# Kernel optimization log

Hardware: AMD Instinct MI355X
Metric: run time of the kernel (lower is better)

The kernel has to match this reference:

```python
import jax, jax.numpy as jnp
import numpy as np

B, S, D = 8, 2048, 512

def setup_inputs() -> dict:
    key = jax.random.key(0)
    ks = jax.random.split(key, 7)
    scale = 1.0 / np.sqrt(D)
    return {
        "x": jax.random.normal(ks[0], (B, S, D), dtype=jnp.float32),
        "Wq": jax.random.normal(ks[1], (D, D), dtype=jnp.float32) * scale,
        "bq": jax.random.normal(ks[2], (D,), dtype=jnp.float32) * 0.01,
        "Wk": jax.random.normal(ks[3], (D, D), dtype=jnp.float32) * scale,
        "bk": jax.random.normal(ks[4], (D,), dtype=jnp.float32) * 0.01,
        "Wv": jax.random.normal(ks[5], (D, D), dtype=jnp.float32) * scale,
        "bv": jax.random.normal(ks[6], (D,), dtype=jnp.float32) * 0.01,
    }

def reference(x, Wq, bq, Wk, bk, Wv, bv):
    # Q/K/V projections: [B,S,D] @ [D,D]
    q = jnp.einsum('bsd,de->bse', x, Wq) + bq
    k = jnp.einsum('bsd,de->bse', x, Wk) + bk
    v = jnp.einsum('bsd,de->bse', x, Wv) + bv
    # NOTE: original module has NO 1/sqrt(d) scaling
    scores = jnp.einsum('bqd,bkd->bqk', q, k)          # [B,S,S]
    attn = jax.nn.softmax(scores, axis=-1)
    return jnp.einsum('bqk,bkd->bqd', attn, v)         # [B,S,D]
```

## Files before the change

kernel.cpp:

```cpp
#include <hip/hip_runtime.h>
#include <hip/hip_fp16.h>


typedef unsigned short u16;
typedef unsigned int u32;
typedef __attribute__((ext_vector_type(8))) _Float16 f16x8;
typedef __attribute__((ext_vector_type(16))) float f32x16;

#define S_LEN 2048
#define D_DIM 512
#define B_N 8

__device__ __forceinline__ u16 f2bf(float f) {
    u32 u = __float_as_uint(f);
    u32 r = u + 0x7FFFu + ((u >> 16) & 1u);
    return (u16)(r >> 16);
}
__device__ __forceinline__ float bf2f(u16 h) {
    return __uint_as_float((u32)h << 16);
}
__device__ __forceinline__ u16 f2h(float f) {
    _Float16 h = (_Float16)f;
    return *(u16*)&h;
}
__device__ __forceinline__ void gl16(const u16* g, u16* l) {
    __builtin_amdgcn_global_load_lds(
        (const __attribute__((address_space(1))) void*)g,
        (__attribute__((address_space(3))) void*)l, 16, 0, 0);
}
__device__ __forceinline__ f32x16 mfma16(f16x8 a, f16x8 b, f32x16 c) {
    return __builtin_amdgcn_mfma_f32_32x32x16_f16(a, b, c, 0, 0, 0);
}

__global__ void detect_k(const u16* __restrict__ x, int* __restrict__ flag)
{
    int t = threadIdx.x;
    u16 u = x[2 * t];
    int e = (u >> 7) & 0xFF;
    int sane = (e == 0) || (e >= 110 && e <= 140);
    unsigned long long b = __ballot(sane);
    if (t == 0) *flag = (__popcll(b) >= 32) ? 1 : 0;
}

__global__ __launch_bounds__(256) void cvt_x(
    const void* __restrict__ X, u16* __restrict__ xf,
    const int* __restrict__ flagp)
{
    const size_t i4 = ((size_t)blockIdx.x * 256 + threadIdx.x) * 4;
    float f[4];
    if (*flagp) {
        ushort4 u = *(const ushort4*)((const u16*)X + i4);
        f[0] = bf2f(u.x); f[1] = bf2f(u.y); f[2] = bf2f(u.z); f[3] = bf2f(u.w);
    } else {
        float4 ff = *(const float4*)((const float*)X + i4);
        f[0] = ff.x; f[1] = ff.y; f[2] = ff.z; f[3] = ff.w;
    }
    ushort4 h;
    h.x = f2h(f[0]); h.y = f2h(f[1]); h.z = f2h(f[2]); h.w = f2h(f[3]);
    *(ushort4*)(xf + i4) = h;
}

__global__ __launch_bounds__(256) void pack_w(
    const void* __restrict__ Wq, const void* __restrict__ Wk, const void* __restrict__ Wv,
    u16* __restrict__ WT, const int* __restrict__ flagp)
{
    const int k = blockIdx.x;
    const int n = blockIdx.y * 256 + threadIdx.x;
    const void* W = n < 512 ? Wq : n < 1024 ? Wk : Wv;
    const int nc = n & 511;
    float f = *flagp ? bf2f(((const u16*)W)[(size_t)k * 512 + nc])
                     : ((const float*)W)[(size_t)k * 512 + nc];
    WT[(size_t)n * 512 + k] = f2h(f);
}

__global__ void pack_bias(
    const void* __restrict__ bq, const void* __restrict__ bk, const void* __restrict__ bv,
    float* __restrict__ bcat, const int* __restrict__ flagp)
{
    const int t = blockIdx.x * 256 + threadIdx.x;
    const void* b = t < 512 ? bq : t < 1024 ? bk : bv;
    const int i = t & 511;
    bcat[t] = *flagp ? bf2f(((const u16*)b)[i]) : ((const float*)b)[i];
}

template <int EPI>
__global__ __launch_bounds__(256) void gemm_f16(
    const u16* __restrict__ A_, const u16* __restrict__ B_,
    void* __restrict__ Cp, const float* __restrict__ biasf,
    u16* __restrict__ Oq, u16* __restrict__ Ok, u16* __restrict__ OvT,
    const int* __restrict__ flagp,
    int K, int lda, int ldb, int ldc, long sA, long sB, long sC, long cbase)
{
    const int tid = threadIdx.x;
    const int lane = tid & 63, wav = tid >> 6;
    const int l31 = lane & 31, lh = lane >> 5;

    int bx, by, bz;
    if constexpr (EPI != 2) {
        const int gx = gridDim.x, gy = gridDim.y;
        const int total = gx * gy * gridDim.z;
        const int chunk = total >> 3;
        int lin = (blockIdx.z * gy + blockIdx.y) * gx + blockIdx.x;
        lin = (lin & 7) * chunk + (lin >> 3);
        bx = lin % gx;
        by = (lin / gx) % gy;
        bz = lin / (gx * gy);
    } else {
        bx = blockIdx.x; by = blockIdx.y; bz = blockIdx.z;
    }

    const int m0 = by * 128, n0 = bx * 128;
    const int bm = (wav >> 1) * 64, bn = (wav & 1) * 64;

    const u16* A = A_ + (size_t)bz * sA;
    const u16* B = B_ + (size_t)bz * sB;

    __shared__ __align__(16) u16 sh[16384];
    u16* As = sh;
    u16* Bs = sh + 8192;

    const int r0 = tid >> 3;
    const int c0 = ((tid & 7) ^ (r0 & 7)) * 8;
    size_t aoff[4], boff[4];
#pragma unroll
    for (int j = 0; j < 4; j++) {
        aoff[j] = (size_t)(m0 + r0 + j * 32) * lda + c0;
        boff[j] = (size_t)(n0 + r0 + j * 32) * ldb + c0;
    }
    const int g7 = l31 & 7;
    const int rowA0 = (bm + l31) * 64, rowA1 = (bm + 32 + l31) * 64;
    const int rowB0 = (bn + l31) * 64, rowB1 = (bn + 32 + l31) * 64;

    f32x16 acc[2][2];
#pragma unroll
    for (int i = 0; i < 2; i++)
#pragma unroll
        for (int j = 0; j < 2; j++)
#pragma unroll
            for (int r = 0; r < 16; r++) acc[i][j][r] = 0.f;

    for (int k0 = 0; k0 < K; k0 += 64) {
#pragma unroll
        for (int j = 0; j < 4; j++) {
            gl16(A + aoff[j] + k0, As + j * 2048 + wav * 512);
            gl16(B + boff[j] + k0, Bs + j * 2048 + wav * 512);
        }
        __syncthreads();

#pragma unroll
        for (int h = 0; h < 4; h++) {
            const int so = ((h * 2 + lh) ^ g7) * 8;
            f16x8 af[2], bfr[2];
            af[0] = *(const f16x8*)&As[rowA0 + so];
            af[1] = *(const f16x8*)&As[rowA1 + so];
            bfr[0] = *(const f16x8*)&Bs[rowB0 + so];
            bfr[1] = *(const f16x8*)&Bs[rowB1 + so];
#pragma unroll
            for (int i = 0; i < 2; i++)
#pragma unroll
                for (int j = 0; j < 2; j++)
                    acc[i][j] = mfma16(af[i], bfr[j], acc[i][j]);
        }
        __syncthreads();
    }

    if (EPI == 2) {
        const int mode = bx >> 2;
        if (mode == 2) {
#pragma unroll
            for (int it = 0; it < 2; it++)
#pragma unroll
                for (int jt = 0; jt < 2; jt++) {
                    const int lc = bn + jt * 32 + l31;
                    const float badd = biasf[n0 + lc];
#pragma unroll
                    for (int r = 0; r < 16; r++) {
                        const int row = bm + it * 32 + (r & 3) + 8 * (r >> 2) + 4 * lh;
                        sh[lc * 128 + (row ^ ((lc & 15) << 3))] =
                            f2h(acc[it][jt][r] + badd);
                    }
                }
            __syncthreads();
            const int vbase = n0 - 1024;
#pragma unroll
            for (int p = 0; p < 8; p++) {
                const int q = p * 256 + tid;
                const int lc = q >> 4, ch = q & 15;
                const int g = ch ^ (lc & 15);
                f16x8 val = *(const f16x8*)&sh[lc * 128 + g * 8];
                *(f16x8*)&OvT[(size_t)(vbase + lc) * 16384 + m0 + ch * 8] = val;
            }
        } else {
#pragma unroll
            for (int it = 0; it < 2; it++)
#pragma unroll
                for (int jt = 0; jt < 2; jt++) {
                    const int gcol = n0 + bn + jt * 32 + l31;
                    const int lcol = gcol & 511;
                    const float badd = biasf[gcol];
#pragma unroll
                    for (int r = 0; r < 16; r++) {
                        const int row = m0 + bm + it * 32 + (r & 3) + 8 * (r >> 2) + 4 * lh;
                        const float v = acc[it][jt][r] + badd;
                        if (mode == 0) Oq[(size_t)row * 512 + lcol] = f2h(v);
                        else           Ok[(size_t)row * 512 + lcol] = f2h(v);
                    }
                }
        }
    } else if (EPI == 0) {
        float* Cf = (float*)Cp;
        const long coff = (long)bz * sC;
#pragma unroll
        for (int it = 0; it < 2; it++)
#pragma unroll
            for (int jt = 0; jt < 2; jt++) {
                const int col = n0 + bn + jt * 32 + l31;
#pragma unroll
                for (int r = 0; r < 16; r++) {
                    const int row = m0 + bm + it * 32 + (r & 3) + 8 * (r >> 2) + 4 * lh;
                    Cf[(size_t)(coff + (long)row * ldc + col)] = acc[it][jt][r];
                }
            }
    } else {
        const int isbf = *flagp;
        float* Cf = (float*)Cp;
        u16* Cb = (u16*)Cp;
        const long coff = cbase + (long)bz * sC;
#pragma unroll
        for (int it = 0; it < 2; it++)
#pragma unroll
            for (int jt = 0; jt < 2; jt++) {
                const int col = n0 + bn + jt * 32 + l31;
#pragma unroll
                for (int r = 0; r < 16; r++) {
                    const int row = m0 + bm + it * 32 + (r & 3) + 8 * (r >> 2) + 4 * lh;
                    const size_t idx = (size_t)(coff + (long)row * ldc + col);
                    if (isbf) Cb[idx] = f2bf(acc[it][jt][r]);
                    else Cf[idx] = acc[it][jt][r];
                }
            }
    }
}

__global__ __launch_bounds__(256) void softmax_k(float* __restrict__ sc)
{
    float* srow = sc + (size_t)blockIdx.x * S_LEN;
    const int tid = threadIdx.x;

    float4 a = ((const float4*)srow)[tid];
    float4 b = ((const float4*)srow)[256 + tid];

    float m = fmaxf(fmaxf(fmaxf(a.x, a.y), fmaxf(a.z, a.w)),
                    fmaxf(fmaxf(b.x, b.y), fmaxf(b.z, b.w)));
#pragma unroll
    for (int off = 32; off > 0; off >>= 1) m = fmaxf(m, __shfl_down(m, off));

    __shared__ float redm[4], reds[4];
    if ((tid & 63) == 0) redm[tid >> 6] = m;
    __syncthreads();
    m = fmaxf(fmaxf(redm[0], redm[1]), fmaxf(redm[2], redm[3]));

    a.x = __expf(a.x - m); a.y = __expf(a.y - m);
    a.z = __expf(a.z - m); a.w = __expf(a.w - m);
    b.x = __expf(b.x - m); b.y = __expf(b.y - m);
    b.z = __expf(b.z - m); b.w = __expf(b.w - m);
    float s = a.x + a.y + a.z + a.w + b.x + b.y + b.z + b.w;
#pragma unroll
    for (int off = 32; off > 0; off >>= 1) s += __shfl_down(s, off);
    if ((tid & 63) == 0) reds[tid >> 6] = s;
    __syncthreads();
    s = reds[0] + reds[1] + reds[2] + reds[3];

    const float inv = 1.0f / s;
    ushort4 pa, pb;
    pa.x = f2h(a.x * inv); pa.y = f2h(a.y * inv);
    pa.z = f2h(a.z * inv); pa.w = f2h(a.w * inv);
    pb.x = f2h(b.x * inv); pb.y = f2h(b.y * inv);
    pb.z = f2h(b.z * inv); pb.w = f2h(b.w * inv);
    ((ushort4*)srow)[tid] = pa;
    ((ushort4*)srow)[256 + tid] = pb;
}

extern "C" void kernel_launch(void* const* d_in, const int* in_sizes, int n_in,
                              void* d_out, int out_size, void* d_ws, size_t ws_size,
                              hipStream_t stream)
{
    const void* x  = d_in[0];
    const void* Wq = d_in[1]; const void* bq = d_in[2];
    const void* Wk = d_in[3]; const void* bk = d_in[4];
    const void* Wv = d_in[5]; const void* bv = d_in[6];

    const int S = S_LEN, D = D_DIM;
    const long SD = (long)S * D;

    char* w = (char*)d_ws;
    int*   flag = (int*)w;
    u16*   WT   = (u16*)(w + 1024);
    float* bcat = (float*)(w + 1573888);
    u16*   xf   = (u16*)(w + 1580032);
    u16*   qf   = (u16*)(w + 18357248);
    u16*   kf   = (u16*)(w + 35134464);
    u16*   vT   = (u16*)(w + 51911680);
    float* scA  = (float*)(w + 68688896);

    const size_t avail = ws_size > 68688896ull ? ws_size - 68688896ull : 0;
    const size_t perb = (size_t)S * S * 4;
    const int c = avail >= 8 * perb ? 8 : avail >= 4 * perb ? 4 : avail >= 2 * perb ? 2 : 1;

    dim3 blk(256);

    detect_k<<<1, 64, 0, stream>>>((const u16*)x, flag);
    cvt_x<<<8192, blk, 0, stream>>>(x, xf, flag);
    pack_w<<<dim3(512, 6), blk, 0, stream>>>(Wq, Wk, Wv, WT, flag);
    pack_bias<<<6, blk, 0, stream>>>(bq, bk, bv, bcat, flag);

    gemm_f16<2><<<dim3(12, 128, 1), blk, 0, stream>>>(
        xf, WT, nullptr, bcat, qf, kf, vT, flag,
        512, 512, 512, 0, 0, 0, 0, 0);

    for (int cb = 0; cb < B_N; cb += c) {
        const size_t off = (size_t)cb * SD;
        gemm_f16<0><<<dim3(16, 16, c), blk, 0, stream>>>(
            qf + off, kf + off, scA, nullptr, nullptr, nullptr, nullptr, flag,
            512, 512, 512, S, SD, SD, (long)S * S, 0);
        softmax_k<<<c * S, blk, 0, stream>>>(scA);
        gemm_f16<1><<<dim3(4, 16, c), blk, 0, stream>>>(
            (const u16*)scA, vT + (size_t)cb * S, d_out, nullptr,
            nullptr, nullptr, nullptr, flag,
            S, 2 * S, B_N * S, D, 2ll * S * S, S, SD, (long)cb * SD);
    }
}
```

Baseline: 274.7 us.

## Replace P·V GEMM with 512-thread triple-buffered 16x16x32 MFMA kernel

Adds a dedicated gemm8pv kernel for the attention-probabilities times V product. It uses 256x128 tiles with 8 waves, triple-buffered LDS stages filled by global_load_lds, and 16x16x32 MFMAs. Global loads are interleaved with the MFMA phases, with explicit waitcnt/barriers and setprio. This is meant to hide load latency and raise MFMA throughput for the largest GEMM. In exchange it uses much more LDS with one block per CU, and fewer blocks (4x8xc), which may limit occupancy.

```diff
diff --git a/kernel.cpp b/kernel.cpp
--- a/kernel.cpp
+++ b/kernel.cpp
@@ -6,6 +6,7 @@
 typedef unsigned int u32;
 typedef __attribute__((ext_vector_type(8))) _Float16 f16x8;
 typedef __attribute__((ext_vector_type(16))) float f32x16;
+typedef __attribute__((ext_vector_type(4))) float f32x4;
 
 #define S_LEN 2048
 #define D_DIM 512
@@ -30,6 +31,9 @@
 }
 __device__ __forceinline__ f32x16 mfma16(f16x8 a, f16x8 b, f32x16 c) {
     return __builtin_amdgcn_mfma_f32_32x32x16_f16(a, b, c, 0, 0, 0);
+}
+__device__ __forceinline__ f32x4 mfma16q(f16x8 a, f16x8 b, f32x4 c) {
+    return __builtin_amdgcn_mfma_f32_16x16x32_f16(a, b, c, 0, 0, 0);
 }
 
 __global__ void detect_k(const u16* __restrict__ x, int* __restrict__ flag)
@@ -207,7 +211,7 @@
                     }
                 }
         }
-    } else if (EPI == 0) {
+    } else {
         float* Cf = (float*)Cp;
         const long coff = (long)bz * sC;
 #pragma unroll
@@ -221,23 +225,164 @@
                     Cf[(size_t)(coff + (long)row * ldc + col)] = acc[it][jt][r];
                 }
             }
-    } else {
-        const int isbf = *flagp;
-        float* Cf = (float*)Cp;
-        u16* Cb = (u16*)Cp;
-        const long coff = cbase + (long)bz * sC;
-#pragma unroll
-        for (int it = 0; it < 2; it++)
-#pragma unroll
-            for (int jt = 0; jt < 2; jt++) {
-                const int col = n0 + bn + jt * 32 + l31;
-#pragma unroll
-                for (int r = 0; r < 16; r++) {
-                    const int row = m0 + bm + it * 32 + (r & 3) + 8 * (r >> 2) + 4 * lh;
-                    const size_t idx = (size_t)(coff + (long)row * ldc + col);
-                    if (isbf) Cb[idx] = f2bf(acc[it][jt][r]);
-                    else Cf[idx] = acc[it][jt][r];
+    }
+}
+
+__global__ __launch_bounds__(512, 1) void gemm8pv(
+    const u16* __restrict__ A_, const u16* __restrict__ B_,
+    void* __restrict__ Cp, const int* __restrict__ flagp,
+    int K, int lda, int ldb, int ldc, long sA, long sB, long sC, long cbase)
+{
+    const int tid = threadIdx.x;
+    const int lane = tid & 63;
+    const int wid = tid >> 6;
+    const int wm = wid >> 2;
+    const int wn = wid & 3;
+    const int l15 = lane & 15, lq = lane >> 4;
+    const int colB = wn * 32;
+
+    const int gx = gridDim.x, gy = gridDim.y;
+    const int total = gx * gy * gridDim.z;
+    const int chunk = total >> 3;
+    int lin = (blockIdx.z * gy + blockIdx.y) * gx + blockIdx.x;
+    lin = (lin & 7) * chunk + (lin >> 3);
+    const int bx = lin % gx;
+    const int by = (lin / gx) % gy;
+    const int bz = lin / (gx * gy);
+
+    const int m0 = by * 256, n0 = bx * 128;
+
+    const u16* A = A_ + (size_t)bz * sA;
+    const u16* B = B_ + (size_t)bz * sB;
+
+    __shared__ __align__(16) u16 As[3][256 * 64];
+    __shared__ __align__(16) u16 Bs[3][128 * 64];
+
+    const int r0 = tid >> 3;
+    const int c0 = ((tid & 7) ^ (r0 & 7)) * 8;
+    u32 aoffs[4], boffs[2];
+#pragma unroll
+    for (int j = 0; j < 4; j++)
+        aoffs[j] = (u32)((m0 + j * 64 + r0) * lda + c0);
+#pragma unroll
+    for (int j = 0; j < 2; j++)
+        boffs[j] = (u32)((n0 + j * 64 + r0) * ldb + c0);
+    const int stageDst = wid << 9;
+
+    const int nt = K >> 6;
+
+    f32x4 acc[8][2];
+#pragma unroll
+    for (int mi = 0; mi < 8; mi++)
+#pragma unroll
+        for (int nj = 0; nj < 2; nj++)
+#pragma unroll
+            for (int r = 0; r < 4; r++) acc[mi][nj][r] = 0.f;
+
+    auto stage6 = [&](u16* dA, u16* dB, int k0) {
+#pragma unroll
+        for (int j = 0; j < 4; j++)
+            gl16(A + aoffs[j] + k0, dA + (j << 12) + stageDst);
+#pragma unroll
+        for (int j = 0; j < 2; j++)
+            gl16(B + boffs[j] + k0, dB + (j << 12) + stageDst);
+    };
+    auto rdA = [&](const u16* buf, int p, int h, int ks) -> f16x8 {
+        const int row = (wm << 7) + (p << 5) + (h << 4) + l15;
+        const int off = (row << 6) + ((((ks << 2) + lq) ^ (row & 7)) << 3);
+        return *(const f16x8*)(buf + off);
+    };
+    auto rdB = [&](const u16* buf, int nj, int ks) -> f16x8 {
+        const int row = colB + (nj << 4) + l15;
+        const int off = (row << 6) + ((((ks << 2) + lq) ^ (row & 7)) << 3);
+        return *(const f16x8*)(buf + off);
+    };
+
+    stage6(As[0], Bs[0], 0);
+    stage6(As[1], Bs[1], 64);
+    asm volatile("s_waitcnt vmcnt(6)" ::: "memory");
+    __builtin_amdgcn_sched_barrier(0);
+    __builtin_amdgcn_s_barrier();
+
+    for (int tt = 0; tt < nt; tt++) {
+        const int bi = tt % 3, si = (tt + 2) % 3;
+        const u16* Ab = As[bi];
+        const u16* Bb = Bs[bi];
+        u16* dA = As[si];
+        u16* dB = Bs[si];
+        const bool doStage = (tt + 2 < nt);
+        const int k2 = (tt + 2) * 64;
+        f16x8 bfr[2][2];
+#pragma unroll
+        for (int p = 0; p < 4; p++) {
+            if (p == 0) {
+#pragma unroll
+                for (int nj = 0; nj < 2; nj++)
+#pragma unroll
+                    for (int ks = 0; ks < 2; ks++)
+                        bfr[nj][ks] = rdB(Bb, nj, ks);
+            }
+            f16x8 a[2][2];
+#pragma unroll
+            for (int h = 0; h < 2; h++)
+#pragma unroll
+                for (int ks = 0; ks < 2; ks++)
+                    a[h][ks] = rdA(Ab, p, h, ks);
+            if (doStage) {
+                if (p == 0) {
+                    gl16(A + aoffs[0] + k2, dA + stageDst);
+                    gl16(A + aoffs[1] + k2, dA + (1 << 12) + stageDst);
+                } else if (p == 1) {
+                    gl16(A + aoffs[2] + k2, dA + (2 << 12) + stageDst);
+                    gl16(A + aoffs[3] + k2, dA + (3 << 12) + stageDst);
+                } else if (p == 2) {
+                    gl16(B + boffs[0] + k2, dB + stageDst);
+                    gl16(B + boffs[1] + k2, dB + (1 << 12) + stageDst);
                 }
+            }
+            if (p == 3) {
+                asm volatile("s_waitcnt lgkmcnt(0)" ::: "memory");
+                __builtin_amdgcn_sched_barrier(0);
+            }
+            __builtin_amdgcn_s_barrier();
+            __builtin_amdgcn_s_setprio(1);
+#pragma unroll
+            for (int h = 0; h < 2; h++)
+#pragma unroll
+                for (int nj = 0; nj < 2; nj++)
+#pragma unroll
+                    for (int ks = 0; ks < 2; ks++)
+                        acc[2 * p + h][nj] =
+                            mfma16q(a[h][ks], bfr[nj][ks], acc[2 * p + h][nj]);
+            __builtin_amdgcn_s_setprio(0);
+            if (p < 3) {
+                __builtin_amdgcn_s_barrier();
+            } else if (tt + 1 < nt) {
+                if (tt + 2 < nt)
+                    asm volatile("s_waitcnt vmcnt(6)" ::: "memory");
+                else
+                    asm volatile("s_waitcnt vmcnt(0)" ::: "memory");
+                __builtin_amdgcn_sched_barrier(0);
+                __builtin_amdgcn_s_barrier();
+            }
+        }
+    }
+
+    const int isbf = *flagp;
+    float* Cf = (float*)Cp;
+    u16* Cb = (u16*)Cp;
+    const long coff = cbase + (long)bz * sC;
+#pragma unroll
+    for (int nj = 0; nj < 2; nj++) {
+        const int col = n0 + colB + nj * 16 + l15;
+#pragma unroll
+        for (int mi = 0; mi < 8; mi++)
+#pragma unroll
+            for (int r = 0; r < 4; r++) {
+                const int row = m0 + (wm << 7) + mi * 16 + lq * 4 + r;
+                const size_t idx = (size_t)(coff + (long)row * ldc + col);
+                if (isbf) Cb[idx] = f2bf(acc[mi][nj][r]);
+                else Cf[idx] = acc[mi][nj][r];
             }
     }
 }
@@ -307,7 +452,7 @@
     const size_t perb = (size_t)S * S * 4;
     const int c = avail >= 8 * perb ? 8 : avail >= 4 * perb ? 4 : avail >= 2 * perb ? 2 : 1;
 
-    dim3 blk(256);
+    dim3 blk(256), blk5(512);
 
     detect_k<<<1, 64, 0, stream>>>((const u16*)x, flag);
     cvt_x<<<8192, blk, 0, stream>>>(x, xf, flag);
@@ -324,9 +469,8 @@
             qf + off, kf + off, scA, nullptr, nullptr, nullptr, nullptr, flag,
             512, 512, 512, S, SD, SD, (long)S * S, 0);
         softmax_k<<<c * S, blk, 0, stream>>>(scA);
-        gemm_f16<1><<<dim3(4, 16, c), blk, 0, stream>>>(
-            (const u16*)scA, vT + (size_t)cb * S, d_out, nullptr,
-            nullptr, nullptr, nullptr, flag,
+        gemm8pv<<<dim3(4, 8, c), blk5, 0, stream>>>(
+            (const u16*)scA, vT + (size_t)cb * S, d_out, flag,
             S, 2 * S, B_N * S, D, 2ll * S * S, S, SD, (long)cb * SD);
     }
 }
```

Measured after the change: 288.5 us. +5.0%, slower.
